# Performance work log

Hardware: AMD Instinct MI355X
Metric: run time of the kernel (lower is better)

Reference implementation:

```python
import jax, jax.numpy as jnp
import numpy as np

N_NODES = 50000
N_EDGES = 800000
NEMBED = 128
HDIM = 256
NCLASS = 40


def setup_inputs() -> dict:
    key = jax.random.key(0)
    ks = jax.random.split(key, 8)
    x = jax.random.normal(ks[0], (N_NODES, NEMBED), dtype=jnp.float32)
    edge_index = jax.random.randint(ks[1], (2, N_EDGES), 0, N_NODES, dtype=jnp.int64)
    # SAGEConv params (PyG: out = lin_l(mean_aggr) + lin_r(x_self), bias on lin_l)
    s1 = 1.0 / np.sqrt(NEMBED)
    W_l = jax.random.uniform(ks[2], (HDIM, NEMBED), minval=-s1, maxval=s1, dtype=jnp.float32)
    b_l = jax.random.uniform(ks[3], (HDIM,), minval=-s1, maxval=s1, dtype=jnp.float32)
    W_r = jax.random.uniform(ks[4], (HDIM, NEMBED), minval=-s1, maxval=s1, dtype=jnp.float32)
    # mlp: weight init normal(std=0.05) per reset_parameters, default bias init
    W_mlp = 0.05 * jax.random.normal(ks[5], (NCLASS, HDIM), dtype=jnp.float32)
    s2 = 1.0 / np.sqrt(HDIM)
    b_mlp = jax.random.uniform(ks[6], (NCLASS,), minval=-s2, maxval=s2, dtype=jnp.float32)
    return {"x": x, "W_l": W_l, "b_l": b_l, "W_r": W_r,
            "W_mlp": W_mlp, "b_mlp": b_mlp, "edge_index": edge_index}


def reference(x, W_l, b_l, W_r, W_mlp, b_mlp, edge_index):
    src, dst = edge_index[0], edge_index[1]
    # mean aggregation of neighbor features: scatter-add then divide by in-degree
    msg = x[src]  # [E, nembed] irregular gather
    agg = jax.ops.segment_sum(msg, dst, num_segments=N_NODES)  # [N, nembed]
    deg = jax.ops.segment_sum(jnp.ones((N_EDGES,), dtype=x.dtype), dst,
                              num_segments=N_NODES)
    mean = agg / jnp.maximum(deg, 1.0)[:, None]
    # SAGEConv: lin_l(mean) + lin_r(x)
    h = mean @ W_l.T + b_l + x @ W_r.T  # [N, hdim]
    h = jax.nn.relu(h)
    # dropout is identity in eval mode
    out = h @ W_mlp.T + b_mlp  # [N, nclass]
    return out
```

## Files before the change

kernel.cpp:

```cpp
#include <hip/hip_runtime.h>

#define N_NODESC 50000
#define NEMBEDC 128
#define HDIMC 256
#define NCLASSC 40
#define NBUCK 196
#define SEGCAP 32
#define BKCAP 4352

typedef short short8v __attribute__((ext_vector_type(8)));
typedef float float4v __attribute__((ext_vector_type(4)));
typedef float float2v __attribute__((ext_vector_type(2)));


__device__ __forceinline__ unsigned rbf(float f) {
  unsigned u = __builtin_bit_cast(unsigned, f);
  return (u + 0x7FFFu + ((u >> 16) & 1u)) >> 16;
}

__global__ __launch_bounds__(512) void k_prep_bucket(
    const float* __restrict__ x, const float* __restrict__ W_l,
    const float* __restrict__ W_r, const float* __restrict__ W_mlp,
    const int* __restrict__ e32, int E,
    unsigned short* __restrict__ xb, unsigned char* __restrict__ x8,
    short* __restrict__ bh, short* __restrict__ wh,
    unsigned char* __restrict__ cnt, unsigned* __restrict__ bbuf) {
  int blk = blockIdx.x;
  int tid = threadIdx.x;
  if (blk < 1563) {
    int i = (blk * 512 + tid) * 8;
    if (i < 6400000) {
      float4 a = *(const float4*)(x + i);
      float4 b = *(const float4*)(x + i + 4);
      float f[8] = {a.x, a.y, a.z, a.w, b.x, b.y, b.z, b.w};
      unsigned h[8];
#pragma unroll
      for (int j = 0; j < 8; ++j) h[j] = rbf(f[j]);
      uint4 o;
      o.x = h[0] | (h[1] << 16);
      o.y = h[2] | (h[3] << 16);
      o.z = h[4] | (h[5] << 16);
      o.w = h[6] | (h[7] << 16);
      *(uint4*)(xb + i) = o;
      int w0 = __builtin_amdgcn_cvt_pk_fp8_f32(f[0], f[1], 0, false);
      w0 = __builtin_amdgcn_cvt_pk_fp8_f32(f[2], f[3], w0, true);
      int w1 = __builtin_amdgcn_cvt_pk_fp8_f32(f[4], f[5], 0, false);
      w1 = __builtin_amdgcn_cvt_pk_fp8_f32(f[6], f[7], w1, true);
      uint2 o8;
      o8.x = (unsigned)w0;
      o8.y = (unsigned)w1;
      *(uint2*)(x8 + i) = o8;
    }
    return;
  }
  if (blk < 1715) {
    int i = (blk - 1563) * 512 + tid;
    if (i < 65536) {
      int e = i & 7, l = (i >> 3) & 63, nf = (i >> 9) & 15, ks = i >> 13;
      int k = ks * 32 + (l >> 4) * 8 + e;
      int n = nf * 16 + (l & 15);
      float v = (k < 128) ? W_l[n * 128 + k] : W_r[n * 128 + (k - 128)];
      bh[i] = (short)rbf(v);
    } else {
      int j = i - 65536;
      int e = j & 7, l = (j >> 3) & 63, g = j >> 9;
      int nf = g % 3, ks = g / 3;
      int k = ks * 32 + (l >> 4) * 8 + e;
      int n = nf * 16 + (l & 15);
      float v = (n < NCLASSC) ? W_mlp[n * HDIMC + k] : 0.f;
      wh[j] = (short)rbf(v);
    }
    return;
  }
  __shared__ int hist[NBUCK];
  __shared__ int s_is32;
  int j = blk - 1715;
  if (tid == 0) s_is32 = 0;
  if (tid < NBUCK) hist[tid] = 0;
  __syncthreads();
  int base = j * 2048;
  {
    int e = base + tid;
    if (e < E && e32[2 * e + 1] != 0) atomicOr(&s_is32, 1);
  }
  __syncthreads();
  int is64 = !s_is32;
  unsigned pe[4];
  int rk[4];
#pragma unroll
  for (int jj = 0; jj < 4; ++jj) {
    int e = base + jj * 512 + tid;
    pe[jj] = 0xFFFFFFFFu;
    rk[jj] = 0;
    if (e < E) {
      int src = is64 ? e32[2 * e] : e32[e];
      int dst = is64 ? e32[2 * E + 2 * e] : e32[E + e];
      pe[jj] = ((unsigned)dst << 16) | (unsigned)src;
      rk[jj] = atomicAdd(&hist[dst >> 8], 1);
    }
  }
  __syncthreads();
  if (tid < NBUCK) {
    int c = hist[tid];
    cnt[j * NBUCK + tid] = (unsigned char)(c < SEGCAP ? c : SEGCAP);
  }
#pragma unroll
  for (int jj = 0; jj < 4; ++jj) {
    if (pe[jj] != 0xFFFFFFFFu && rk[jj] < SEGCAP) {
      int b = pe[jj] >> 24;
      bbuf[(j * NBUCK + b) * SEGCAP + rk[jj]] = pe[jj];
    }
  }
}

__global__ __launch_bounds__(1024) void k_bsort(
    const unsigned* __restrict__ bbuf, const unsigned char* __restrict__ cnt,
    int nseg, int* __restrict__ deg, int* __restrict__ offs,
    unsigned short* __restrict__ csr16) {
  __shared__ int hist[256];
  __shared__ int off[256];
  __shared__ int cur[256];
  __shared__ unsigned char scnt[400];
  int tid = threadIdx.x;
  int b = blockIdx.x;
  if (tid < 256) hist[tid] = 0;
  for (int j = tid; j < nseg; j += 1024) scnt[j] = cnt[j * NBUCK + b];
  __syncthreads();
  int nslot = nseg * SEGCAP;
  for (int i = tid; i < nslot; i += 1024) {
    int j = i >> 5, slot = i & 31;
    if (slot < (int)scnt[j]) {
      unsigned pe = bbuf[(j * NBUCK + b) * SEGCAP + slot];
      atomicAdd(&hist[(pe >> 16) & 255], 1);
    }
  }
  __syncthreads();
  if (tid < 256) off[tid] = hist[tid];
  __syncthreads();
  for (int d = 1; d < 256; d <<= 1) {
    int t = (tid < 256 && tid >= d) ? off[tid - d] : 0;
    __syncthreads();
    if (tid < 256) off[tid] += t;
    __syncthreads();
  }
  if (tid < 256) {
    int ex = off[tid] - hist[tid];
    int dstart = ex < BKCAP ? ex : BKCAP;
    int dend = (ex + hist[tid]) < BKCAP ? (ex + hist[tid]) : BKCAP;
    int n = (b << 8) + tid;
    deg[n] = dend - dstart;
    offs[n] = b * BKCAP + dstart;
    cur[tid] = ex;
  }
  __syncthreads();
  for (int i = tid; i < nslot; i += 1024) {
    int j = i >> 5, slot = i & 31;
    if (slot < (int)scnt[j]) {
      unsigned pe = bbuf[(j * NBUCK + b) * SEGCAP + slot];
      int ln = (pe >> 16) & 255;
      int p = atomicAdd(&cur[ln], 1);
      if (p < BKCAP) csr16[b * BKCAP + p] = (unsigned short)(pe & 0xFFFFu);
    }
  }
}

__global__ __launch_bounds__(512, 8) void k_aggregate_bf8(
    const unsigned char* __restrict__ x8, const unsigned short* __restrict__ csr16,
    const int* __restrict__ offs, const int* __restrict__ deg,
    unsigned* __restrict__ meanb32) {
  int wave = threadIdx.x >> 6;
  int lane = threadIdx.x & 63;
  int node = blockIdx.x * 8 + wave;
  if (node >= N_NODESC) return;
  int beg = __builtin_amdgcn_readfirstlane(offs[node]);
  int d = __builtin_amdgcn_readfirstlane(deg[node]);
  int q = lane >> 4;
  int ql = lane & 15;
  const uint2* x2 = (const uint2*)x8;
  float acc[8];
#pragma unroll
  for (int i = 0; i < 8; ++i) acc[i] = 0.f;
#define DECODE_ADD(v)                                                     \
  {                                                                       \
    float2v p0 = __builtin_amdgcn_cvt_pk_f32_fp8((int)(v).x, false);      \
    float2v p1 = __builtin_amdgcn_cvt_pk_f32_fp8((int)(v).x, true);       \
    float2v p2 = __builtin_amdgcn_cvt_pk_f32_fp8((int)(v).y, false);      \
    float2v p3 = __builtin_amdgcn_cvt_pk_f32_fp8((int)(v).y, true);       \
    acc[0] += p0.x; acc[1] += p0.y; acc[2] += p1.x; acc[3] += p1.y;       \
    acc[4] += p2.x; acc[5] += p2.y; acc[6] += p3.x; acc[7] += p3.y;       \
  }
  int e = 0;
  for (; e + 16 <= d; e += 16) {
    int s0 = csr16[beg + e + q];
    int s1 = csr16[beg + e + 4 + q];
    int s2 = csr16[beg + e + 8 + q];
    int s3 = csr16[beg + e + 12 + q];
    uint2 v0 = x2[s0 * 16 + ql];
    uint2 v1 = x2[s1 * 16 + ql];
    uint2 v2 = x2[s2 * 16 + ql];
    uint2 v3 = x2[s3 * 16 + ql];
    DECODE_ADD(v0) DECODE_ADD(v1) DECODE_ADD(v2) DECODE_ADD(v3)
  }
  if (e + 8 <= d) {
    int s0 = csr16[beg + e + q];
    int s1 = csr16[beg + e + 4 + q];
    uint2 v0 = x2[s0 * 16 + ql];
    uint2 v1 = x2[s1 * 16 + ql];
    DECODE_ADD(v0) DECODE_ADD(v1)
    e += 8;
  }
  if (e + 4 <= d) {
    int s0 = csr16[beg + e + q];
    uint2 v0 = x2[s0 * 16 + ql];
    DECODE_ADD(v0)
    e += 4;
  }
  if (e < d) {
    int r = d - e;
    if (q < r) {
      int s0 = csr16[beg + e + q];
      uint2 v0 = x2[s0 * 16 + ql];
      DECODE_ADD(v0)
    }
  }
#undef DECODE_ADD
#pragma unroll
  for (int i = 0; i < 8; ++i) {
    acc[i] += __shfl_xor(acc[i], 16);
    acc[i] += __shfl_xor(acc[i], 32);
  }
  if (lane < 16) {
    float inv = 1.0f / (float)(d > 0 ? d : 1);
    uint4 o;
    o.x = rbf(acc[0] * inv) | (rbf(acc[1] * inv) << 16);
    o.y = rbf(acc[2] * inv) | (rbf(acc[3] * inv) << 16);
    o.z = rbf(acc[4] * inv) | (rbf(acc[5] * inv) << 16);
    o.w = rbf(acc[6] * inv) | (rbf(acc[7] * inv) << 16);
    ((uint4*)(meanb32 + (size_t)node * 64))[lane] = o;
  }
}

__global__ __launch_bounds__(512, 6) void k_fused_mfma(
    const unsigned short* __restrict__ meanb, const unsigned short* __restrict__ xb,
    const short* __restrict__ bmh, const short* __restrict__ wmh,
    const float* __restrict__ b_l, const float* __restrict__ b_mlp,
    float* __restrict__ out) {
  __shared__ short sh[16384];
  int t = threadIdx.x;
  int m0 = blockIdx.x * 64;

#pragma unroll
  for (int r = 0; r < 4; ++r) {
    int c = t + 512 * r;
    int row = c >> 5;
    int kc = (c & 31) ^ (row & 7);
    int node = m0 + row;
    const unsigned short* src = (kc < 16) ? (meanb + (size_t)node * 128 + kc * 8)
                                          : (xb + (size_t)node * 128 + (kc - 16) * 8);
    __builtin_amdgcn_global_load_lds(
        (const __attribute__((address_space(1))) unsigned int*)src,
        (__attribute__((address_space(3))) unsigned int*)&sh[c * 8],
        16, 0, 0);
  }
  __syncthreads();

  int w = t >> 6, l = t & 63;
  int lr = l & 15, lg = l >> 4;

  float4v acc[4][2];
#pragma unroll
  for (int mi = 0; mi < 4; ++mi)
#pragma unroll
    for (int nj = 0; nj < 2; ++nj) acc[mi][nj] = (float4v){0.f, 0.f, 0.f, 0.f};

  for (int ks = 0; ks < 8; ++ks) {
    short8v a[4];
#pragma unroll
    for (int mi = 0; mi < 4; ++mi) {
      int row = mi * 16 + lr;
      int kc = ks * 4 + lg;
      a[mi] = *(short8v*)&sh[row * 256 + ((kc ^ (row & 7)) << 3)];
    }
    short8v bh4[2];
#pragma unroll
    for (int nj = 0; nj < 2; ++nj) {
      int fi = ((ks * 16 + w * 2 + nj) * 64 + l) * 8;
      bh4[nj] = *(const short8v*)&bmh[fi];
    }
#pragma unroll
    for (int mi = 0; mi < 4; ++mi)
#pragma unroll
      for (int nj = 0; nj < 2; ++nj)
        acc[mi][nj] = __builtin_amdgcn_mfma_f32_16x16x32_bf16(a[mi], bh4[nj], acc[mi][nj], 0, 0, 0);
  }
  __syncthreads();

#pragma unroll
  for (int mi = 0; mi < 4; ++mi)
#pragma unroll
    for (int nj = 0; nj < 2; ++nj) {
      int col = (w * 2 + nj) * 16 + lr;
      float bb = b_l[col];
      int kc2 = col >> 3;
#pragma unroll
      for (int r = 0; r < 4; ++r) {
        int row = mi * 16 + lg * 4 + r;
        float v = fmaxf(acc[mi][nj][r] + bb, 0.f);
        sh[row * 256 + ((kc2 ^ (row & 7)) << 3) + (col & 7)] = (short)rbf(v);
      }
    }
  __syncthreads();

  int mf = w & 3;
  float4v a2[2];
  a2[0] = (float4v){0.f, 0.f, 0.f, 0.f};
  a2[1] = a2[0];
  for (int ks = 0; ks < 8; ++ks) {
    int row = mf * 16 + lr;
    int kc = ks * 4 + lg;
    short8v hh = *(short8v*)&sh[row * 256 + ((kc ^ (row & 7)) << 3)];
#pragma unroll
    for (int u = 0; u < 2; ++u) {
      if (w >= 4 && u > 0) break;
      int nf = (w < 4) ? u : 2;
      int fi = ((ks * 3 + nf) * 64 + l) * 8;
      short8v wh8 = *(const short8v*)&wmh[fi];
      a2[u] = __builtin_amdgcn_mfma_f32_16x16x32_bf16(hh, wh8, a2[u], 0, 0, 0);
    }
  }
#pragma unroll
  for (int u = 0; u < 2; ++u) {
    if (w >= 4 && u > 0) break;
    int nf = (w < 4) ? u : 2;
    int col = nf * 16 + lr;
    if (col < NCLASSC) {
      float bb = b_mlp[col];
#pragma unroll
      for (int r = 0; r < 4; ++r) {
        int node = m0 + mf * 16 + lg * 4 + r;
        if (node < N_NODESC) out[node * NCLASSC + col] = a2[u][r] + bb;
      }
    }
  }
}

extern "C" void kernel_launch(void* const* d_in, const int* in_sizes, int n_in,
                              void* d_out, int out_size, void* d_ws, size_t ws_size,
                              hipStream_t stream) {
  const float* x     = (const float*)d_in[0];
  const float* W_l   = (const float*)d_in[1];
  const float* b_l   = (const float*)d_in[2];
  const float* W_r   = (const float*)d_in[3];
  const float* W_mlp = (const float*)d_in[4];
  const float* b_mlp = (const float*)d_in[5];
  const int*   e32   = (const int*)d_in[6];
  int E = in_sizes[6] / 2;
  float* out = (float*)d_out;

  char* ws = (char*)d_ws;
  int* deg         = (int*)(ws + 4096);
  int* offs        = (int*)(ws + 204800);
  short* wmh       = (short*)(ws + 405504);
  short* bmh       = (short*)(ws + 458752);
  unsigned char* cnt = (unsigned char*)(ws + 602112);
  unsigned short* csr16 = (unsigned short*)(ws + 720896);
  unsigned* bbuf   = (unsigned*)(ws + 2427904);
  unsigned short* meanb = (unsigned short*)(ws + 2427904);
  unsigned short* xb = (unsigned short*)(ws + 15228928);
  unsigned char* x8  = (unsigned char*)(ws + 28028928);

  int nseg = (E + 2047) / 2048;
  k_prep_bucket<<<1715 + nseg, 512, 0, stream>>>(x, W_l, W_r, W_mlp, e32, E, xb, x8,
                                                 bmh, wmh, cnt, bbuf);
  k_bsort<<<NBUCK, 1024, 0, stream>>>(bbuf, cnt, nseg, deg, offs, csr16);
  k_aggregate_bf8<<<6250, 512, 0, stream>>>(x8, csr16, offs, deg, (unsigned*)meanb);
  k_fused_mfma<<<782, 512, 0, stream>>>(meanb, xb, bmh, wmh, b_l, b_mlp, out);
}
```

Measured before the change: 79.36 us.

## Double-buffer LDS tiles so each fused-MFMA block processes two row tiles

Each block of the fused MFMA kernel now handles two 64-row tiles using two LDS buffers. The second tile's global-to-LDS loads are issued before the first tile is computed, so load latency can overlap with MFMA work. The grid is halved and the launch-bounds occupancy hint drops from 6 to 4. LDS per block doubles, which lowers resident blocks per CU and leaves fewer blocks overall, so the overlap may not beat the latency hiding that higher occupancy already gave.

New measurement: 84.95 us. 1.07x slower.

```diff
diff --git a/kernel.cpp b/kernel.cpp
--- a/kernel.cpp
+++ b/kernel.cpp
@@ -240,108 +240,122 @@
   }
 }
 
-__global__ __launch_bounds__(512, 6) void k_fused_mfma(
+__global__ __launch_bounds__(512, 4) void k_fused_mfma(
     const unsigned short* __restrict__ meanb, const unsigned short* __restrict__ xb,
     const short* __restrict__ bmh, const short* __restrict__ wmh,
     const float* __restrict__ b_l, const float* __restrict__ b_mlp,
     float* __restrict__ out) {
-  __shared__ short sh[16384];
+  __shared__ short sh[2][16384];
   int t = threadIdx.x;
-  int m0 = blockIdx.x * 64;
-
-#pragma unroll
-  for (int r = 0; r < 4; ++r) {
-    int c = t + 512 * r;
-    int row = c >> 5;
-    int kc = (c & 31) ^ (row & 7);
-    int node = m0 + row;
-    const unsigned short* src = (kc < 16) ? (meanb + (size_t)node * 128 + kc * 8)
-                                          : (xb + (size_t)node * 128 + (kc - 16) * 8);
-    __builtin_amdgcn_global_load_lds(
-        (const __attribute__((address_space(1))) unsigned int*)src,
-        (__attribute__((address_space(3))) unsigned int*)&sh[c * 8],
-        16, 0, 0);
-  }
-  __syncthreads();
-
   int w = t >> 6, l = t & 63;
   int lr = l & 15, lg = l >> 4;
 
-  float4v acc[4][2];
-#pragma unroll
-  for (int mi = 0; mi < 4; ++mi)
-#pragma unroll
-    for (int nj = 0; nj < 2; ++nj) acc[mi][nj] = (float4v){0.f, 0.f, 0.f, 0.f};
-
-  for (int ks = 0; ks < 8; ++ks) {
-    short8v a[4];
-#pragma unroll
-    for (int mi = 0; mi < 4; ++mi) {
-      int row = mi * 16 + lr;
-      int kc = ks * 4 + lg;
-      a[mi] = *(short8v*)&sh[row * 256 + ((kc ^ (row & 7)) << 3)];
-    }
-    short8v bh4[2];
-#pragma unroll
-    for (int nj = 0; nj < 2; ++nj) {
-      int fi = ((ks * 16 + w * 2 + nj) * 64 + l) * 8;
-      bh4[nj] = *(const short8v*)&bmh[fi];
-    }
-#pragma unroll
-    for (int mi = 0; mi < 4; ++mi)
-#pragma unroll
-      for (int nj = 0; nj < 2; ++nj)
-        acc[mi][nj] = __builtin_amdgcn_mfma_f32_16x16x32_bf16(a[mi], bh4[nj], acc[mi][nj], 0, 0, 0);
-  }
-  __syncthreads();
-
-#pragma unroll
-  for (int mi = 0; mi < 4; ++mi)
-#pragma unroll
-    for (int nj = 0; nj < 2; ++nj) {
-      int col = (w * 2 + nj) * 16 + lr;
-      float bb = b_l[col];
-      int kc2 = col >> 3;
-#pragma unroll
-      for (int r = 0; r < 4; ++r) {
-        int row = mi * 16 + lg * 4 + r;
-        float v = fmaxf(acc[mi][nj][r] + bb, 0.f);
-        sh[row * 256 + ((kc2 ^ (row & 7)) << 3) + (col & 7)] = (short)rbf(v);
-      }
-    }
-  __syncthreads();
-
-  int mf = w & 3;
-  float4v a2[2];
-  a2[0] = (float4v){0.f, 0.f, 0.f, 0.f};
-  a2[1] = a2[0];
-  for (int ks = 0; ks < 8; ++ks) {
-    int row = mf * 16 + lr;
-    int kc = ks * 4 + lg;
-    short8v hh = *(short8v*)&sh[row * 256 + ((kc ^ (row & 7)) << 3)];
-#pragma unroll
-    for (int u = 0; u < 2; ++u) {
-      if (w >= 4 && u > 0) break;
-      int nf = (w < 4) ? u : 2;
-      int fi = ((ks * 3 + nf) * 64 + l) * 8;
-      short8v wh8 = *(const short8v*)&wmh[fi];
-      a2[u] = __builtin_amdgcn_mfma_f32_16x16x32_bf16(hh, wh8, a2[u], 0, 0, 0);
-    }
-  }
-#pragma unroll
-  for (int u = 0; u < 2; ++u) {
-    if (w >= 4 && u > 0) break;
-    int nf = (w < 4) ? u : 2;
-    int col = nf * 16 + lr;
-    if (col < NCLASSC) {
-      float bb = b_mlp[col];
-#pragma unroll
-      for (int r = 0; r < 4; ++r) {
-        int node = m0 + mf * 16 + lg * 4 + r;
-        if (node < N_NODESC) out[node * NCLASSC + col] = a2[u][r] + bb;
-      }
-    }
-  }
+#define STAGE(buf, mbase)                                                      \
+  {                                                                            \
+    _Pragma("unroll")                                                          \
+    for (int r = 0; r < 4; ++r) {                                              \
+      int c = t + 512 * r;                                                     \
+      int row = c >> 5;                                                        \
+      int kc = (c & 31) ^ (row & 7);                                           \
+      int node = (mbase) + row;                                                \
+      const unsigned short* src =                                              \
+          (kc < 16) ? (meanb + (size_t)node * 128 + kc * 8)                    \
+                    : (xb + (size_t)node * 128 + (kc - 16) * 8);               \
+      __builtin_amdgcn_global_load_lds(                                        \
+          (const __attribute__((address_space(1))) unsigned int*)src,          \
+          (__attribute__((address_space(3))) unsigned int*)&sh[buf][c * 8],    \
+          16, 0, 0);                                                           \
+    }                                                                          \
+  }
+
+#define COMPUTE(buf, mbase)                                                    \
+  {                                                                            \
+    float4v acc[4][2];                                                         \
+    _Pragma("unroll")                                                          \
+    for (int mi = 0; mi < 4; ++mi)                                             \
+      _Pragma("unroll")                                                        \
+      for (int nj = 0; nj < 2; ++nj) acc[mi][nj] = (float4v){0.f,0.f,0.f,0.f}; \
+    for (int ks = 0; ks < 8; ++ks) {                                           \
+      short8v a[4];                                                            \
+      _Pragma("unroll")                                                        \
+      for (int mi = 0; mi < 4; ++mi) {                                         \
+        int row = mi * 16 + lr;                                                \
+        int kc = ks * 4 + lg;                                                  \
+        a[mi] = *(short8v*)&sh[buf][row * 256 + ((kc ^ (row & 7)) << 3)];      \
+      }                                                                        \
+      short8v bh4[2];                                                          \
+      _Pragma("unroll")                                                        \
+      for (int nj = 0; nj < 2; ++nj) {                                         \
+        int fi = ((ks * 16 + w * 2 + nj) * 64 + l) * 8;                        \
+        bh4[nj] = *(const short8v*)&bmh[fi];                                   \
+      }                                                                        \
+      _Pragma("unroll")                                                        \
+      for (int mi = 0; mi < 4; ++mi)                                           \
+        _Pragma("unroll")                                                      \
+        for (int nj = 0; nj < 2; ++nj)                                         \
+          acc[mi][nj] = __builtin_amdgcn_mfma_f32_16x16x32_bf16(               \
+              a[mi], bh4[nj], acc[mi][nj], 0, 0, 0);                           \
+    }                                                                          \
+    __syncthreads();               \
+    _Pragma("unroll")                                                          \
+    for (int mi = 0; mi < 4; ++mi)                                             \
+      _Pragma("unroll")                                                        \
+      for (int nj = 0; nj < 2; ++nj) {                                         \
+        int col = (w * 2 + nj) * 16 + lr;                                      \
+        float bb = b_l[col];                                                   \
+        int kc2 = col >> 3;                                                    \
+        _Pragma("unroll")                                                      \
+        for (int r = 0; r < 4; ++r) {                                          \
+          int row = mi * 16 + lg * 4 + r;                                      \
+          float v = fmaxf(acc[mi][nj][r] + bb, 0.f);                           \
+          sh[buf][row * 256 + ((kc2 ^ (row & 7)) << 3) + (col & 7)] =          \
+              (short)rbf(v);                                                   \
+        }                                                                      \
+      }                                                                        \
+    __syncthreads();                                                           \
+    int mf = w & 3;                                                            \
+    float4v a2[2];                                                             \
+    a2[0] = (float4v){0.f, 0.f, 0.f, 0.f};                                     \
+    a2[1] = a2[0];                                                             \
+    for (int ks = 0; ks < 8; ++ks) {                                           \
+      int row = mf * 16 + lr;                                                  \
+      int kc = ks * 4 + lg;                                                    \
+      short8v hh = *(short8v*)&sh[buf][row * 256 + ((kc ^ (row & 7)) << 3)];   \
+      _Pragma("unroll")                                                        \
+      for (int u = 0; u < 2; ++u) {                                            \
+        if (w >= 4 && u > 0) break;                                            \
+        int nf = (w < 4) ? u : 2;                                              \
+        int fi = ((ks * 3 + nf) * 64 + l) * 8;                                 \
+        short8v wh8 = *(const short8v*)&wmh[fi];                               \
+        a2[u] = __builtin_amdgcn_mfma_f32_16x16x32_bf16(hh, wh8, a2[u],        \
+                                                        0, 0, 0);              \
+      }                                                                        \
+    }                                                                          \
+    _Pragma("unroll")                                                          \
+    for (int u = 0; u < 2; ++u) {                                              \
+      if (w >= 4 && u > 0) break;                                              \
+      int nf = (w < 4) ? u : 2;                                                \
+      int col = nf * 16 + lr;                                                  \
+      if (col < NCLASSC) {                                                     \
+        float bb = b_mlp[col];                                                 \
+        _Pragma("unroll")                                                      \
+        for (int r = 0; r < 4; ++r) {                                          \
+          int node = (mbase) + mf * 16 + lg * 4 + r;                           \
+          if (node < N_NODESC) out[node * NCLASSC + col] = a2[u][r] + bb;      \
+        }                                                                      \
+      }                                                                        \
+    }                                                                          \
+  }
+
+  int m0 = blockIdx.x * 128;
+  STAGE(0, m0)
+  __syncthreads();
+  STAGE(1, m0 + 64)
+  COMPUTE(0, m0)
+  __syncthreads();
+  COMPUTE(1, m0 + 64)
+#undef STAGE
+#undef COMPUTE
 }
 
 extern "C" void kernel_launch(void* const* d_in, const int* in_sizes, int n_in,
@@ -374,5 +388,5 @@
                                                  bmh, wmh, cnt, bbuf);
   k_bsort<<<NBUCK, 1024, 0, stream>>>(bbuf, cnt, nseg, deg, offs, csr16);
   k_aggregate_bf8<<<6250, 512, 0, stream>>>(x8, csr16, offs, deg, (unsigned*)meanb);
-  k_fused_mfma<<<782, 512, 0, stream>>>(meanb, xb, bmh, wmh, b_l, b_mlp, out);
-}
+  k_fused_mfma<<<391, 512, 0, stream>>>(meanb, xb, bmh, wmh, b_l, b_mlp, out);
+}
```
